# Performance work log

Hardware: AMD Instinct MI355X
Metric: run time of the kernel (lower is better)

Reference implementation:

```python
import jax, jax.numpy as jnp
import numpy as np

B, Q, C, M = 32, 4096, 91, 512
T_MAX = 256          # track ids in [0, T_MAX]; 0 = invalid
SENT = T_MAX + 1     # sentinel segment for invalid preds
NSEG = T_MAX + 2
IMG_W, IMG_H = 1920.0, 1080.0
SCALE = 1.0 / float(np.sqrt(IMG_W ** 2 + IMG_H ** 2))
IOU_THR = 0.5
A_TRACK, A_SPAT, A_TEMP = 2.0, 1.5, 1.8
B_FP, B_FN, G_SW = 0.9, 0.9, 1.5


def _make_boxes(key, shape):
    k1, k2 = jax.random.split(key)
    xy = jax.random.uniform(k1, shape[:-1] + (2,)) * jnp.array([IMG_W - 220.0, IMG_H - 220.0])
    wh = jax.random.uniform(k2, shape[:-1] + (2,)) * 200.0 + 4.0
    return jnp.concatenate([xy, xy + wh], axis=-1)


def setup_inputs() -> dict:
    key = jax.random.key(0)
    ks = jax.random.split(key, 5)
    return {
        'pred_boxes': _make_boxes(ks[0], (B, Q, 4)),
        'pred_logits': jax.random.normal(ks[1], (B, Q, C), dtype=jnp.float32),
        'track_ids': jax.random.randint(ks[2], (B, Q), 0, T_MAX + 1, dtype=jnp.int32),
        'gt_boxes': _make_boxes(ks[3], (B, M, 4)),
        'gt_track_ids': jax.random.randint(ks[4], (B, M), 1, T_MAX + 1, dtype=jnp.int32),
    }


def _box_iou(b1, b2):
    a1 = jnp.clip(b1[:, 2] - b1[:, 0], 0.0) * jnp.clip(b1[:, 3] - b1[:, 1], 0.0)
    a2 = jnp.clip(b2[:, 2] - b2[:, 0], 0.0) * jnp.clip(b2[:, 3] - b2[:, 1], 0.0)
    lt = jnp.maximum(b1[:, None, :2], b2[None, :, :2])
    rb = jnp.minimum(b1[:, None, 2:], b2[None, :, 2:])
    wh = jnp.clip(rb - lt, 0.0)
    inter = wh[..., 0] * wh[..., 1]
    iou = inter / (a1[:, None] + a2[None, :] - inter + 1e-6)
    return jnp.clip(iou, 0.0, 1.0)


def _per_batch(pb, pid, gb, gid):
    valid = pid > 0
    seg = jnp.where(valid, pid, SENT)              # invalid preds -> sentinel bucket
    ar = jnp.arange(NSEG)
    real = (ar > 0) & (ar <= T_MAX)
    ious = _box_iou(pb, gb)                        # (Q, M)

    gt_cnt = jax.ops.segment_sum(jnp.ones(M, jnp.float32), gid, NSEG)
    gt_present = gt_cnt > 0
    pred_cnt = jax.ops.segment_sum(jnp.ones(Q, jnp.float32), seg, NSEG)
    pred_present = (pred_cnt > 0) & real

    # ---- tracking loss ----
    fn_loss = B_FN * jnp.sum(jnp.where(gt_present & ~pred_present, gt_cnt, 0.0))
    match = pid[:, None] == gid[None, :]           # (Q, M)
    max_iou = jnp.max(jnp.where(match, ious, -1.0), axis=1)
    loc_mask = valid & gt_present[pid]
    loc = jnp.sum(jnp.where(loc_mask, 1.0 - max_iou, 0.0))
    wrong = (ious > IOU_THR) & valid[:, None] & ~match & pred_present[gid][None, :]
    switch = G_SW * jnp.sum(wrong.astype(jnp.float32))
    fp_loss = B_FP * jnp.sum(jnp.where(valid & ~gt_present[pid], 1.0, 0.0))
    tracking = fn_loss + loc + switch + fp_loss

    # ---- spatial consistency (per-track mean abs deviation of w, h) ----
    w = pb[:, 2] - pb[:, 0]
    h = pb[:, 3] - pb[:, 1]
    safe_cnt = jnp.maximum(pred_cnt, 1.0)
    mw = jax.ops.segment_sum(w, seg, NSEG) / safe_cnt
    mh = jax.ops.segment_sum(h, seg, NSEG) / safe_cnt
    dev_w = jnp.abs(w - mw[seg]) * SCALE
    dev_h = jnp.abs(h - mh[seg]) * SCALE
    mdw = jax.ops.segment_sum(dev_w, seg, NSEG) / safe_cnt
    mdh = jax.ops.segment_sum(dev_h, seg, NSEG) / safe_cnt
    n_unique = jnp.sum(((pred_cnt > 0) & real).astype(jnp.float32))
    sp_ok = (pred_cnt > 1) & real
    spatial = jnp.sum(jnp.where(sp_ok, mdw + mdh, 0.0)) / jnp.maximum(n_unique, 1.0)
    nvalid = jnp.sum(valid.astype(jnp.float32))
    spatial = jnp.where(nvalid > 1, spatial, 0.0)

    # ---- temporal consistency (per-track second-difference of centers) ----
    order = jnp.argsort(seg, stable=True)          # stable: preserves query order per track
    s_id = seg[order]
    centers = jnp.stack([(pb[:, 0] + pb[:, 2]) * 0.5, (pb[:, 1] + pb[:, 3]) * 0.5], axis=1)
    s_c = centers[order]
    vel = s_c[1:] - s_c[:-1]
    same1 = (s_id[1:] == s_id[:-1]) & (s_id[1:] <= T_MAX)
    acc = (vel[1:] - vel[:-1]) * SCALE
    same2 = same1[1:] & same1[:-1]
    sq = jnp.sum(acc * acc, axis=1)
    acc_norm = jnp.where(same2, jnp.sqrt(jnp.maximum(sq, 1e-30)), 0.0)
    sum_acc = jax.ops.segment_sum(acc_norm, s_id[2:], NSEG)
    te_ok = (pred_cnt > 2) & real
    temporal = jnp.sum(jnp.where(te_ok, sum_acc / jnp.maximum(pred_cnt - 2.0, 1.0), 0.0))
    temporal = temporal / jnp.maximum(n_unique, 1.0)
    temporal = jnp.where(nvalid > 1, temporal, 0.0)

    z = (nvalid > 0).astype(jnp.float32)           # torch code skips batches with no valid preds
    return tracking * z, spatial * z, temporal * z, n_unique * z


def reference(pred_boxes, pred_logits, track_ids, gt_boxes, gt_track_ids):
    tr, sp, te, nu = jax.vmap(_per_batch)(pred_boxes, track_ids, gt_boxes, gt_track_ids)
    nt = jnp.sum(nu)
    denom = jnp.maximum(nt, 1.0)
    lt = jnp.where(nt > 0, jnp.sum(tr) / denom, 0.0)
    ls = jnp.where(nt > 0, jnp.sum(sp) / denom, 0.0)
    lte = jnp.where(nt > 0, jnp.sum(te) / denom, 0.0)
    san = lambda x: jnp.where(jnp.isfinite(x), x, 0.0)
    lt, ls, lte = san(lt), san(ls), san(lte)
    total = san(A_TRACK * lt + A_SPAT * ls + A_TEMP * lte)
    # [loss_unitrack, loss_unitrack_tracking, loss_unitrack_spatial, loss_unitrack_temporal]
    return jnp.stack([total, lt, ls, lte])
```

## Files before the change

### kernel.cpp

```cpp
#include <hip/hip_runtime.h>
#include <math.h>

#define NB 32
#define NQ 4096
#define NM 512
#define NT 256
#define NSENT 257
#define NSEGS 258
#define HP 33
#define NXB 64
#define XBW (1.0f/30.0f)
#define WMAX 204.0f

__device__ __forceinline__ float scale_const() {
  return 1.0f / sqrtf(1920.0f * 1920.0f + 1080.0f * 1080.0f);
}

__global__ __launch_bounds__(1024) void k_stats(
    const float4* __restrict__ pred_boxes,
    const int*    __restrict__ track_ids,
    const float4* __restrict__ gt_boxes,
    const int*    __restrict__ gt_ids,
    float*        __restrict__ acc,
    float4*       __restrict__ e_box,
    float*        __restrict__ e_meta,
    unsigned short* __restrict__ qord,
    int*          __restrict__ g_boff)
{
  const int b    = blockIdx.x;
  const int tid  = threadIdx.x;
  const int lane = tid & 63;
  const int wid  = tid >> 6;
  const float SCALE = scale_const();

  __shared__ unsigned int hist32[NSEGS * HP];
  __shared__ float2 wh_s[NQ];
  __shared__ float2 ct_s[NQ];
  __shared__ __attribute__((aligned(16))) float4 gbox_s[NM];
  __shared__ float  gsa_s[NM];
  __shared__ float  gsa3_s[NM];
  __shared__ unsigned short gt_list[NM];
  __shared__ int gcnt_i[NSEGS], pcnt_i[NSEGS], offs[NSEGS], goffs[NSEGS], cur[NSEGS];
  __shared__ float ppw[NSEGS], gpw[NSEGS];
  __shared__ int qbh[NXB], qbo[NXB], qbc[NXB];
  __shared__ int gbh[NXB], gbo[NXB + 1], gbc[NXB];
  __shared__ float slots[16][8];

  for (int i = tid; i < NSEGS * HP; i += 1024) hist32[i] = 0u;
  if (tid < NSEGS) { gcnt_i[tid] = 0; cur[tid] = 0; }
  if (tid < NXB)   { qbh[tid] = 0; qbc[tid] = 0; gbh[tid] = 0; gbc[tid] = 0; }
  __syncthreads();

  float4 pbox[4]; int segr[4]; int xbr[4];
  #pragma unroll
  for (int k = 0; k < 4; ++k) {
    int q = tid + (k << 10);
    pbox[k] = pred_boxes[b * NQ + q];
    int pid = track_ids[b * NQ + q];
    segr[k] = pid > 0 ? pid : NSENT;
    int xb = (int)(pbox[k].x * XBW); xb = xb > 63 ? 63 : (xb < 0 ? 0 : xb);
    xbr[k] = xb;
    atomicAdd(&qbh[xb], 1);
  }
  float4 gtbox = make_float4(0.f, 0.f, 0.f, 0.f);
  int gtid = 0, gxb = 0;
  float gsa3v = 0.f;
  if (tid < NM) {
    gtbox = gt_boxes[b * NM + tid];
    gtid  = gt_ids[b * NM + tid];
    atomicAdd(&gcnt_i[gtid], 1);
    float sa = fmaxf(gtbox.z - gtbox.x, 0.f) * fmaxf(gtbox.w - gtbox.y, 0.f) + 1e-6f;
    gsa3v = sa * (1.0f / 3.0f);
    gbox_s[tid] = gtbox;
    gsa_s[tid]  = sa;
    gsa3_s[tid] = gsa3v;
    gxb = (int)(gtbox.x * XBW); gxb = gxb > 63 ? 63 : (gxb < 0 ? 0 : gxb);
    atomicAdd(&gbh[gxb], 1);
  }

  int rankr[4];
  #pragma unroll
  for (int k = 0; k < 4; ++k) {
    int seg = segr[k];
    unsigned long long mask = ~0ull;
    #pragma unroll
    for (int bit = 0; bit < 9; ++bit) {
      unsigned long long vote = __ballot((seg >> bit) & 1);
      mask &= ((seg >> bit) & 1) ? vote : ~vote;
    }
    rankr[k] = __popcll(mask & ((1ull << lane) - 1ull));
    if (rankr[k] == 0 && seg != NSENT) {
      int q = tid + (k << 10);
      ((unsigned short*)hist32)[seg * (2 * HP) + (q >> 6)] = (unsigned short)__popcll(mask);
    }
  }
  __syncthreads();

  if (tid < NSEGS) {
    int s = 0;
    #pragma unroll 8
    for (int c2 = 0; c2 < 32; ++c2) {
      unsigned u = hist32[tid * HP + c2];
      s += (int)(u & 0xffffu) + (int)(u >> 16);
    }
    pcnt_i[tid] = s;
    ppw[tid] = (tid >= 1 && tid <= NT && s > 0) ? 1.f : 0.f;
    gpw[tid] = (gcnt_i[tid] > 0) ? 1.f : 0.f;
  }
  if (wid == 14) {
    int v = qbh[lane], sc = v;
    #pragma unroll
    for (int d = 1; d < 64; d <<= 1) { int u = __shfl_up(sc, d); if (lane >= d) sc += u; }
    qbo[lane] = sc - v;
  } else if (wid == 15) {
    int v = gbh[lane], sc = v;
    #pragma unroll
    for (int d = 1; d < 64; d <<= 1) { int u = __shfl_up(sc, d); if (lane >= d) sc += u; }
    int ex = sc - v;
    gbo[lane] = ex;
    g_boff[b * 65 + lane] = ex;
    if (lane == 63) { gbo[64] = sc; g_boff[b * 65 + 64] = sc; }
  }
  __syncthreads();

  if (wid < 2) {
    const int* src = wid ? gcnt_i : pcnt_i;
    int* dst = wid ? goffs : offs;
    int base = lane * 5;
    int v0=0,v1=0,v2=0,v3=0,v4=0;
    if (base + 0 < NSEGS) v0 = src[base + 0];
    if (base + 1 < NSEGS) v1 = src[base + 1];
    if (base + 2 < NSEGS) v2 = src[base + 2];
    if (base + 3 < NSEGS) v3 = src[base + 3];
    if (base + 4 < NSEGS) v4 = src[base + 4];
    int tot = v0 + v1 + v2 + v3 + v4;
    int sc = tot;
    #pragma unroll
    for (int d = 1; d < 64; d <<= 1) { int u = __shfl_up(sc, d); if (lane >= d) sc += u; }
    int run = sc - tot;
    if (base + 0 < NSEGS) { dst[base + 0] = run; run += v0; }
    if (base + 1 < NSEGS) { dst[base + 1] = run; run += v1; }
    if (base + 2 < NSEGS) { dst[base + 2] = run; run += v2; }
    if (base + 3 < NSEGS) { dst[base + 3] = run; run += v3; }
    if (base + 4 < NSEGS) { dst[base + 4] = run; run += v4; }
  }
  __syncthreads();

  if (tid < NSEGS) {
    int run = offs[tid];
    #pragma unroll 8
    for (int c2 = 0; c2 < 32; ++c2) {
      unsigned u = hist32[tid * HP + c2];
      int lo = (int)(u & 0xffffu), hi = (int)(u >> 16);
      hist32[tid * HP + c2] = (unsigned)run | ((unsigned)(run + lo) << 16);
      run += lo + hi;
    }
  }
  __syncthreads();

  float nv_local = 0.f;
  #pragma unroll
  for (int k = 0; k < 4; ++k) {
    int seg = segr[k];
    int q = tid + (k << 10);
    if (seg != NSENT) {
      nv_local += 1.f;
      int c = q >> 6;
      unsigned pr = hist32[seg * HP + (c >> 1)];
      int base = (c & 1) ? (int)(pr >> 16) : (int)(pr & 0xffffu);
      int pos = base + rankr[k];
      float4 bx = pbox[k];
      wh_s[pos] = make_float2(bx.z - bx.x, bx.w - bx.y);
      ct_s[pos] = make_float2((bx.x + bx.z) * 0.5f, (bx.y + bx.w) * 0.5f);
    }
    int xb = xbr[k];
    int qp = qbo[xb] + atomicAdd(&qbc[xb], 1);
    qord[b * NQ + qp] = (unsigned short)q;
  }
  if (tid < NM) {
    int gp = gbo[gxb] + atomicAdd(&gbc[gxb], 1);
    e_box[b * NM + gp]  = gtbox;
    e_meta[b * NM + gp] = (ppw[gtid] > 0.f) ? gsa3v : 3.0e38f;
    int p = atomicAdd(&cur[gtid], 1);
    gt_list[goffs[gtid] + p] = (unsigned short)tid;
  }
  __syncthreads();

  float loc_local = 0.f, mo_local = 0.f;
  #pragma unroll
  for (int k = 0; k < 4; ++k) {
    int seg = segr[k];
    if (seg != NSENT && gpw[seg] > 0.f) {
      float4 p = pbox[k];
      float pa  = fmaxf(p.z - p.x, 0.f) * fmaxf(p.w - p.y, 0.f);
      float pa3 = pa * (1.0f / 3.0f);
      int s0 = goffs[seg], n = gcnt_i[seg];
      float mx = -1.f;
      for (int i = 0; i < n; ++i) {
        int m = gt_list[s0 + i];
        float4 g = gbox_s[m];
        float ix = fmaxf(fminf(p.z, g.z) - fmaxf(p.x, g.x), 0.f);
        float iy = fmaxf(fminf(p.w, g.w) - fmaxf(p.y, g.y), 0.f);
        float inter = ix * iy;
        float iou = inter / (pa + gsa_s[m] - inter);
        mx = fmaxf(mx, fminf(fmaxf(iou, 0.f), 1.f));
        if (inter > pa3 + gsa3_s[m]) mo_local += 1.f;
      }
      loc_local += 1.f - mx;
    }
  }

  float fn_l = 0.f, fp_l = 0.f, sp_l = 0.f, te_l = 0.f, nu_l = 0.f;
  if (tid >= 1 && tid <= NT) {
    int n = pcnt_i[tid], gc = gcnt_i[tid], o = offs[tid];
    if (gc > 0 && n == 0) fn_l = (float)gc;
    if (n > 0) {
      nu_l = 1.f;
      if (gc == 0) fp_l = (float)n;
    }
    if (n > 1) {
      float sumw = 0.f, sumh = 0.f;
      for (int i = 0; i < n; ++i) { float2 w = wh_s[o + i]; sumw += w.x; sumh += w.y; }
      float inv = 1.f / (float)n;
      float mw = sumw * inv, mh = sumh * inv;
      float dw = 0.f, dh = 0.f;
      for (int i = 0; i < n; ++i) {
        float2 w = wh_s[o + i];
        dw += fabsf(w.x - mw) * SCALE;
        dh += fabsf(w.y - mh) * SCALE;
      }
      sp_l = dw * inv + dh * inv;
      if (n > 2) {
        float2 c0 = ct_s[o], c1 = ct_s[o + 1];
        float s = 0.f;
        for (int i = 2; i < n; ++i) {
          float2 c2v = ct_s[o + i];
          float ax = (c2v.x - 2.f * c1.x + c0.x) * SCALE;
          float ay = (c2v.y - 2.f * c1.y + c0.y) * SCALE;
          s += sqrtf(fmaxf(ax * ax + ay * ay, 1e-30f));
          c0 = c1; c1 = c2v;
        }
        te_l = s / (float)(n - 2);
      }
    }
  }

  float vals[8] = {fn_l, fp_l, sp_l, te_l, nu_l, nv_local, loc_local, mo_local};
  #pragma unroll
  for (int j = 0; j < 8; ++j) {
    float v = vals[j];
    #pragma unroll
    for (int off = 32; off; off >>= 1) v += __shfl_down(v, off);
    if (lane == 0) slots[wid][j] = v;
  }
  __syncthreads();
  if (tid < 8) {
    float s = 0.f;
    #pragma unroll
    for (int w = 0; w < 16; ++w) s += slots[w][tid];
    if (tid == 7) s = -s;
    acc[b * 8 + tid] = s;
  }
}

__global__ __launch_bounds__(256) void k_iou(
    const float4* __restrict__ pred_boxes,
    const int*    __restrict__ track_ids,
    const unsigned short* __restrict__ qord,
    const float4* __restrict__ e_box,
    const float*  __restrict__ e_meta,
    const int*    __restrict__ g_boff,
    float*        __restrict__ acc)
{
  const int b    = blockIdx.y;
  const int tid  = threadIdx.x;
  const int slot = blockIdx.x * 256 + tid;
  __shared__ __attribute__((aligned(16))) float4 eb[NM];
  __shared__ float em[NM];
  __shared__ int   bo[NXB + 1];
  __shared__ float redw[4];

  eb[tid]       = e_box[b * NM + tid];
  eb[tid + 256] = e_box[b * NM + tid + 256];
  em[tid]       = e_meta[b * NM + tid];
  em[tid + 256] = e_meta[b * NM + tid + 256];
  if (tid <= NXB) bo[tid] = g_boff[b * 65 + tid];
  __syncthreads();

  int qi = qord[b * NQ + slot];
  float4 p = pred_boxes[b * NQ + qi];
  int pid  = track_ids[b * NQ + qi];
  float pa3 = fmaxf(p.z - p.x, 0.f) * fmaxf(p.w - p.y, 0.f) * (1.0f / 3.0f);

  float x0 = p.x, x1 = p.z;
  #pragma unroll
  for (int off = 32; off; off >>= 1) {
    x0 = fminf(x0, __shfl_xor(x0, off));
    x1 = fmaxf(x1, __shfl_xor(x1, off));
  }
  int lb = (int)(fmaxf(x0 - WMAX, 0.f) * XBW); lb = lb > 63 ? 63 : lb;
  int hb = (int)(fmaxf(x1, 0.f) * XBW);        hb = hb > 63 ? 63 : hb;
  int ms = __builtin_amdgcn_readfirstlane(bo[lb]);
  int me = __builtin_amdgcn_readfirstlane(bo[hb + 1]);

  float wr = 0.f;
  #pragma unroll 4
  for (int m = ms; m < me; ++m) {
    float4 g = eb[m];
    float ix = fmaxf(fminf(p.z, g.z) - fmaxf(p.x, g.x), 0.f);
    float iy = fmaxf(fminf(p.w, g.w) - fmaxf(p.y, g.y), 0.f);
    float inter = ix * iy;
    wr += (inter > pa3 + em[m]) ? 1.f : 0.f;
  }
  if (pid <= 0) wr = 0.f;

  #pragma unroll
  for (int off = 32; off; off >>= 1) wr += __shfl_down(wr, off);
  if ((tid & 63) == 0) redw[tid >> 6] = wr;
  __syncthreads();
  if (tid == 0) {
    float s = redw[0] + redw[1] + redw[2] + redw[3];
    if (s != 0.f) atomicAdd(&acc[b * 8 + 7], s);
  }
}

__global__ __launch_bounds__(64) void k_final(const float* __restrict__ acc, float* __restrict__ out)
{
  const int tid = threadIdx.x;
  float tr = 0.f, sp = 0.f, te = 0.f, nu = 0.f;
  if (tid < NB) {
    const float* a = acc + tid * 8;
    float nvalid = a[5];
    if (nvalid > 0.f) {
      tr = 0.9f * a[0] + a[6] + 1.5f * a[7] + 0.9f * a[1];
      nu = a[4];
      if (nvalid > 1.f) {
        float inu = 1.f / fmaxf(nu, 1.f);
        sp = a[2] * inu;
        te = a[3] * inu;
      }
    }
  }
  #pragma unroll
  for (int off = 32; off; off >>= 1) {
    tr += __shfl_down(tr, off);
    sp += __shfl_down(sp, off);
    te += __shfl_down(te, off);
    nu += __shfl_down(nu, off);
  }
  if (tid == 0) {
    float nt = nu;
    float denom = fmaxf(nt, 1.f);
    float lt  = (nt > 0.f) ? tr / denom : 0.f;
    float ls  = (nt > 0.f) ? sp / denom : 0.f;
    float lte = (nt > 0.f) ? te / denom : 0.f;
    if (!isfinite(lt))  lt  = 0.f;
    if (!isfinite(ls))  ls  = 0.f;
    if (!isfinite(lte)) lte = 0.f;
    float total = 2.0f * lt + 1.5f * ls + 1.8f * lte;
    if (!isfinite(total)) total = 0.f;
    out[0] = total; out[1] = lt; out[2] = ls; out[3] = lte;
  }
}

extern "C" void kernel_launch(void* const* d_in, const int* in_sizes, int n_in,
                              void* d_out, int out_size, void* d_ws, size_t ws_size,
                              hipStream_t stream) {
  const float4* pred_boxes = (const float4*)d_in[0];
  const int*    track_ids  = (const int*)d_in[2];
  const float4* gt_boxes   = (const float4*)d_in[3];
  const int*    gt_ids     = (const int*)d_in[4];
  float* out = (float*)d_out;

  char* w = (char*)d_ws;
  float*          acc    = (float*)w;                      w += 1024;
  float4*         e_box  = (float4*)w;                     w += NB * NM * sizeof(float4);
  float*          e_meta = (float*)w;                      w += NB * NM * sizeof(float);
  unsigned short* qord   = (unsigned short*)w;             w += NB * NQ * sizeof(unsigned short);
  int*            g_boff = (int*)w;

  k_stats<<<NB, 1024, 0, stream>>>(pred_boxes, track_ids, gt_boxes, gt_ids, acc,
                                   e_box, e_meta, qord, g_boff);
  k_iou<<<dim3(NQ / 256, NB), 256, 0, stream>>>(pred_boxes, track_ids, qord,
                                                e_box, e_meta, g_boff, acc);
  k_final<<<1, 64, 0, stream>>>(acc, out);
}
```

Baseline: 39.93 us.

## Move matched-IoU loss into sweep kernel and fuse final reduction via last-block

The per-track matched-IoU (localisation) loop moves out of the single-block-per-batch stats kernel and into the x-binned IoU sweep. Each pred box now computes its max IoU against same-id GT boxes alongside the mostly-overlap count, tagging GT entries with their id so matches are excluded from the overlap term. Pred x-bin ordering now uses ballot-based ranking instead of shared atomics. The separate final kernel is replaced by a last-block-done pattern with a global counter and fences, which saves a launch but adds atomics and a workspace counter that must be reset each call.

```diff
diff --git a/kernel.cpp b/kernel.cpp
--- a/kernel.cpp
+++ b/kernel.cpp
@@ -8,6 +8,7 @@
 #define NSENT 257
 #define NSEGS 258
 #define HP 33
+#define HPX 33
 #define NXB 64
 #define XBW (1.0f/30.0f)
 #define WMAX 204.0f
@@ -23,9 +24,12 @@
     const int*    __restrict__ gt_ids,
     float*        __restrict__ acc,
     float4*       __restrict__ e_box,
-    float*        __restrict__ e_meta,
+    float2*       __restrict__ e_pair,
+    float*        __restrict__ e_sa,
     unsigned short* __restrict__ qord,
-    int*          __restrict__ g_boff)
+    int*          __restrict__ g_boff,
+    unsigned char* __restrict__ gpres,
+    unsigned int* __restrict__ ctr)
 {
   const int b    = blockIdx.x;
   const int tid  = threadIdx.x;
@@ -34,65 +38,69 @@
   const float SCALE = scale_const();
 
   __shared__ unsigned int hist32[NSEGS * HP];
+  __shared__ unsigned int histx[NXB * HPX];
   __shared__ float2 wh_s[NQ];
   __shared__ float2 ct_s[NQ];
-  __shared__ __attribute__((aligned(16))) float4 gbox_s[NM];
-  __shared__ float  gsa_s[NM];
-  __shared__ float  gsa3_s[NM];
-  __shared__ unsigned short gt_list[NM];
-  __shared__ int gcnt_i[NSEGS], pcnt_i[NSEGS], offs[NSEGS], goffs[NSEGS], cur[NSEGS];
-  __shared__ float ppw[NSEGS], gpw[NSEGS];
-  __shared__ int qbh[NXB], qbo[NXB], qbc[NXB];
-  __shared__ int gbh[NXB], gbo[NXB + 1], gbc[NXB];
+  __shared__ int   gcnt_i[NSEGS], pcnt_i[NSEGS], offs[NSEGS];
+  __shared__ float ppw[NSEGS];
+  __shared__ int   qbo[NXB], gbo[NXB + 1], gbc[NXB], gbh[NXB];
   __shared__ float slots[16][8];
 
   for (int i = tid; i < NSEGS * HP; i += 1024) hist32[i] = 0u;
-  if (tid < NSEGS) { gcnt_i[tid] = 0; cur[tid] = 0; }
-  if (tid < NXB)   { qbh[tid] = 0; qbc[tid] = 0; gbh[tid] = 0; gbc[tid] = 0; }
-  __syncthreads();
-
-  float4 pbox[4]; int segr[4]; int xbr[4];
+  for (int i = tid; i < NXB * HPX; i += 1024) histx[i] = 0u;
+  if (tid < NSEGS) gcnt_i[tid] = 0;
+  if (tid < NXB) { gbc[tid] = 0; gbh[tid] = 0; }
+  if (b == 0 && tid == 0) *ctr = 0u;
+  __syncthreads();
+
+  float4 pbox[4]; int segr[4], xbr[4];
+  float nv_local = 0.f;
   #pragma unroll
   for (int k = 0; k < 4; ++k) {
     int q = tid + (k << 10);
     pbox[k] = pred_boxes[b * NQ + q];
     int pid = track_ids[b * NQ + q];
     segr[k] = pid > 0 ? pid : NSENT;
+    if (pid > 0) nv_local += 1.f;
     int xb = (int)(pbox[k].x * XBW); xb = xb > 63 ? 63 : (xb < 0 ? 0 : xb);
     xbr[k] = xb;
-    atomicAdd(&qbh[xb], 1);
   }
   float4 gtbox = make_float4(0.f, 0.f, 0.f, 0.f);
-  int gtid = 0, gxb = 0;
-  float gsa3v = 0.f;
+  int gtid = 0, gxb = 0; float sa = 0.f, sa3 = 0.f;
   if (tid < NM) {
     gtbox = gt_boxes[b * NM + tid];
     gtid  = gt_ids[b * NM + tid];
     atomicAdd(&gcnt_i[gtid], 1);
-    float sa = fmaxf(gtbox.z - gtbox.x, 0.f) * fmaxf(gtbox.w - gtbox.y, 0.f) + 1e-6f;
-    gsa3v = sa * (1.0f / 3.0f);
-    gbox_s[tid] = gtbox;
-    gsa_s[tid]  = sa;
-    gsa3_s[tid] = gsa3v;
+    sa  = fmaxf(gtbox.z - gtbox.x, 0.f) * fmaxf(gtbox.w - gtbox.y, 0.f) + 1e-6f;
+    sa3 = sa * (1.0f / 3.0f);
     gxb = (int)(gtbox.x * XBW); gxb = gxb > 63 ? 63 : (gxb < 0 ? 0 : gxb);
     atomicAdd(&gbh[gxb], 1);
   }
 
-  int rankr[4];
+  int rankr[4], rankx[4];
   #pragma unroll
   for (int k = 0; k < 4; ++k) {
+    int q = tid + (k << 10);
     int seg = segr[k];
-    unsigned long long mask = ~0ull;
+    unsigned long long m1 = ~0ull;
     #pragma unroll
     for (int bit = 0; bit < 9; ++bit) {
       unsigned long long vote = __ballot((seg >> bit) & 1);
-      mask &= ((seg >> bit) & 1) ? vote : ~vote;
-    }
-    rankr[k] = __popcll(mask & ((1ull << lane) - 1ull));
-    if (rankr[k] == 0 && seg != NSENT) {
-      int q = tid + (k << 10);
-      ((unsigned short*)hist32)[seg * (2 * HP) + (q >> 6)] = (unsigned short)__popcll(mask);
-    }
+      m1 &= ((seg >> bit) & 1) ? vote : ~vote;
+    }
+    rankr[k] = __popcll(m1 & ((1ull << lane) - 1ull));
+    if (rankr[k] == 0 && seg != NSENT)
+      ((unsigned short*)hist32)[seg * (2 * HP) + (q >> 6)] = (unsigned short)__popcll(m1);
+    int xb = xbr[k];
+    unsigned long long m2 = ~0ull;
+    #pragma unroll
+    for (int bit = 0; bit < 6; ++bit) {
+      unsigned long long vote = __ballot((xb >> bit) & 1);
+      m2 &= ((xb >> bit) & 1) ? vote : ~vote;
+    }
+    rankx[k] = __popcll(m2 & ((1ull << lane) - 1ull));
+    if (rankx[k] == 0)
+      ((unsigned short*)histx)[xb * (2 * HPX) + (q >> 6)] = (unsigned short)__popcll(m2);
   }
   __syncthreads();
 
@@ -105,13 +113,18 @@
     }
     pcnt_i[tid] = s;
     ppw[tid] = (tid >= 1 && tid <= NT && s > 0) ? 1.f : 0.f;
-    gpw[tid] = (gcnt_i[tid] > 0) ? 1.f : 0.f;
   }
   if (wid == 14) {
-    int v = qbh[lane], sc = v;
+    int s = 0;
+    #pragma unroll 8
+    for (int c2 = 0; c2 < 32; ++c2) {
+      unsigned u = histx[lane * HPX + c2];
+      s += (int)(u & 0xffffu) + (int)(u >> 16);
+    }
+    int sc = s;
     #pragma unroll
     for (int d = 1; d < 64; d <<= 1) { int u = __shfl_up(sc, d); if (lane >= d) sc += u; }
-    qbo[lane] = sc - v;
+    qbo[lane] = sc - s;
   } else if (wid == 15) {
     int v = gbh[lane], sc = v;
     #pragma unroll
@@ -123,26 +136,33 @@
   }
   __syncthreads();
 
-  if (wid < 2) {
-    const int* src = wid ? gcnt_i : pcnt_i;
-    int* dst = wid ? goffs : offs;
+  if (wid == 0) {
     int base = lane * 5;
     int v0=0,v1=0,v2=0,v3=0,v4=0;
-    if (base + 0 < NSEGS) v0 = src[base + 0];
-    if (base + 1 < NSEGS) v1 = src[base + 1];
-    if (base + 2 < NSEGS) v2 = src[base + 2];
-    if (base + 3 < NSEGS) v3 = src[base + 3];
-    if (base + 4 < NSEGS) v4 = src[base + 4];
+    if (base + 0 < NSEGS) v0 = pcnt_i[base + 0];
+    if (base + 1 < NSEGS) v1 = pcnt_i[base + 1];
+    if (base + 2 < NSEGS) v2 = pcnt_i[base + 2];
+    if (base + 3 < NSEGS) v3 = pcnt_i[base + 3];
+    if (base + 4 < NSEGS) v4 = pcnt_i[base + 4];
     int tot = v0 + v1 + v2 + v3 + v4;
     int sc = tot;
     #pragma unroll
     for (int d = 1; d < 64; d <<= 1) { int u = __shfl_up(sc, d); if (lane >= d) sc += u; }
     int run = sc - tot;
-    if (base + 0 < NSEGS) { dst[base + 0] = run; run += v0; }
-    if (base + 1 < NSEGS) { dst[base + 1] = run; run += v1; }
-    if (base + 2 < NSEGS) { dst[base + 2] = run; run += v2; }
-    if (base + 3 < NSEGS) { dst[base + 3] = run; run += v3; }
-    if (base + 4 < NSEGS) { dst[base + 4] = run; run += v4; }
+    if (base + 0 < NSEGS) { offs[base + 0] = run; run += v0; }
+    if (base + 1 < NSEGS) { offs[base + 1] = run; run += v1; }
+    if (base + 2 < NSEGS) { offs[base + 2] = run; run += v2; }
+    if (base + 3 < NSEGS) { offs[base + 3] = run; run += v3; }
+    if (base + 4 < NSEGS) { offs[base + 4] = run; run += v4; }
+  } else if (wid == 13) {
+    int run = qbo[lane];
+    #pragma unroll 8
+    for (int c2 = 0; c2 < 32; ++c2) {
+      unsigned u = histx[lane * HPX + c2];
+      int lo = (int)(u & 0xffffu), hi = (int)(u >> 16);
+      histx[lane * HPX + c2] = (unsigned)run | ((unsigned)(run + lo) << 16);
+      run += lo + hi;
+    }
   }
   __syncthreads();
 
@@ -158,14 +178,12 @@
   }
   __syncthreads();
 
-  float nv_local = 0.f;
   #pragma unroll
   for (int k = 0; k < 4; ++k) {
+    int q = tid + (k << 10);
+    int c = q >> 6;
     int seg = segr[k];
-    int q = tid + (k << 10);
     if (seg != NSENT) {
-      nv_local += 1.f;
-      int c = q >> 6;
       unsigned pr = hist32[seg * HP + (c >> 1)];
       int base = (c & 1) ? (int)(pr >> 16) : (int)(pr & 0xffffu);
       int pos = base + rankr[k];
@@ -173,42 +191,18 @@
       wh_s[pos] = make_float2(bx.z - bx.x, bx.w - bx.y);
       ct_s[pos] = make_float2((bx.x + bx.z) * 0.5f, (bx.y + bx.w) * 0.5f);
     }
-    int xb = xbr[k];
-    int qp = qbo[xb] + atomicAdd(&qbc[xb], 1);
-    qord[b * NQ + qp] = (unsigned short)q;
+    unsigned px = histx[xbr[k] * HPX + (c >> 1)];
+    int xbase = (c & 1) ? (int)(px >> 16) : (int)(px & 0xffffu);
+    qord[b * NQ + xbase + rankx[k]] = (unsigned short)q;
   }
   if (tid < NM) {
     int gp = gbo[gxb] + atomicAdd(&gbc[gxb], 1);
     e_box[b * NM + gp]  = gtbox;
-    e_meta[b * NM + gp] = (ppw[gtid] > 0.f) ? gsa3v : 3.0e38f;
-    int p = atomicAdd(&cur[gtid], 1);
-    gt_list[goffs[gtid] + p] = (unsigned short)tid;
-  }
-  __syncthreads();
-
-  float loc_local = 0.f, mo_local = 0.f;
-  #pragma unroll
-  for (int k = 0; k < 4; ++k) {
-    int seg = segr[k];
-    if (seg != NSENT && gpw[seg] > 0.f) {
-      float4 p = pbox[k];
-      float pa  = fmaxf(p.z - p.x, 0.f) * fmaxf(p.w - p.y, 0.f);
-      float pa3 = pa * (1.0f / 3.0f);
-      int s0 = goffs[seg], n = gcnt_i[seg];
-      float mx = -1.f;
-      for (int i = 0; i < n; ++i) {
-        int m = gt_list[s0 + i];
-        float4 g = gbox_s[m];
-        float ix = fmaxf(fminf(p.z, g.z) - fmaxf(p.x, g.x), 0.f);
-        float iy = fmaxf(fminf(p.w, g.w) - fmaxf(p.y, g.y), 0.f);
-        float inter = ix * iy;
-        float iou = inter / (pa + gsa_s[m] - inter);
-        mx = fmaxf(mx, fminf(fmaxf(iou, 0.f), 1.f));
-        if (inter > pa3 + gsa3_s[m]) mo_local += 1.f;
-      }
-      loc_local += 1.f - mx;
-    }
-  }
+    e_pair[b * NM + gp] = make_float2((ppw[gtid] > 0.f) ? sa3 : 3.0e38f, (float)gtid);
+    e_sa[b * NM + gp]   = sa;
+  }
+  if (tid < NSEGS) gpres[b * NSEGS + tid] = (gcnt_i[tid] > 0) ? 1 : 0;
+  __syncthreads();
 
   float fn_l = 0.f, fp_l = 0.f, sp_l = 0.f, te_l = 0.f, nu_l = 0.f;
   if (tid >= 1 && tid <= NT) {
@@ -245,7 +239,7 @@
     }
   }
 
-  float vals[8] = {fn_l, fp_l, sp_l, te_l, nu_l, nv_local, loc_local, mo_local};
+  float vals[8] = {fn_l, fp_l, sp_l, te_l, nu_l, nv_local, 0.f, 0.f};
   #pragma unroll
   for (int j = 0; j < 8; ++j) {
     float v = vals[j];
@@ -258,7 +252,6 @@
     float s = 0.f;
     #pragma unroll
     for (int w = 0; w < 16; ++w) s += slots[w][tid];
-    if (tid == 7) s = -s;
     acc[b * 8 + tid] = s;
   }
 }
@@ -268,29 +261,43 @@
     const int*    __restrict__ track_ids,
     const unsigned short* __restrict__ qord,
     const float4* __restrict__ e_box,
-    const float*  __restrict__ e_meta,
+    const float2* __restrict__ e_pair,
+    const float*  __restrict__ e_sa,
     const int*    __restrict__ g_boff,
-    float*        __restrict__ acc)
+    const unsigned char* __restrict__ gpres,
+    float*        __restrict__ acc,
+    float*        __restrict__ loc_part,
+    unsigned int* __restrict__ ctr,
+    float*        __restrict__ out)
 {
-  const int b    = blockIdx.y;
-  const int tid  = threadIdx.x;
-  const int slot = blockIdx.x * 256 + tid;
+  const int b   = blockIdx.y;
+  const int bx  = blockIdx.x;
+  const int tid = threadIdx.x;
   __shared__ __attribute__((aligned(16))) float4 eb[NM];
-  __shared__ float em[NM];
-  __shared__ int   bo[NXB + 1];
-  __shared__ float redw[4];
-
-  eb[tid]       = e_box[b * NM + tid];
-  eb[tid + 256] = e_box[b * NM + tid + 256];
-  em[tid]       = e_meta[b * NM + tid];
-  em[tid + 256] = e_meta[b * NM + tid + 256];
+  __shared__ float2 eg[NM];
+  __shared__ float  esa[NM];
+  __shared__ int    bo[NXB + 1];
+  __shared__ float  redl[4], redw[4];
+  __shared__ unsigned last_flag;
+
+  #pragma unroll
+  for (int i = 0; i < 2; ++i) {
+    int m = tid + (i << 8);
+    eb[m]  = e_box[b * NM + m];
+    eg[m]  = e_pair[b * NM + m];
+    esa[m] = e_sa[b * NM + m];
+  }
   if (tid <= NXB) bo[tid] = g_boff[b * 65 + tid];
   __syncthreads();
 
+  const int slot = bx * 256 + tid;
   int qi = qord[b * NQ + slot];
   float4 p = pred_boxes[b * NQ + qi];
   int pid  = track_ids[b * NQ + qi];
-  float pa3 = fmaxf(p.z - p.x, 0.f) * fmaxf(p.w - p.y, 0.f) * (1.0f / 3.0f);
+  float pidf = (float)pid;
+  float pa  = fmaxf(p.z - p.x, 0.f) * fmaxf(p.w - p.y, 0.f);
+  float pa3 = pa * (1.0f / 3.0f);
+  int gp = gpres[b * NSEGS + (pid > 0 ? pid : 0)];
 
   float x0 = p.x, x1 = p.z;
   #pragma unroll
@@ -303,63 +310,84 @@
   int ms = __builtin_amdgcn_readfirstlane(bo[lb]);
   int me = __builtin_amdgcn_readfirstlane(bo[hb + 1]);
 
-  float wr = 0.f;
-  #pragma unroll 4
+  float wr = 0.f, mx = 0.f;
+  #pragma unroll 2
   for (int m = ms; m < me; ++m) {
-    float4 g = eb[m];
+    float4 g  = eb[m];
+    float2 e  = eg[m];
     float ix = fmaxf(fminf(p.z, g.z) - fmaxf(p.x, g.x), 0.f);
     float iy = fmaxf(fminf(p.w, g.w) - fmaxf(p.y, g.y), 0.f);
     float inter = ix * iy;
-    wr += (inter > pa3 + em[m]) ? 1.f : 0.f;
-  }
+    wr += ((inter > pa3 + e.x) && (e.y != pidf)) ? 1.f : 0.f;
+    if (e.y == pidf) {
+      float iou = inter / (pa + esa[m] - inter);
+      mx = fmaxf(mx, fminf(fmaxf(iou, 0.f), 1.f));
+    }
+  }
+  float loc = (pid > 0 && gp) ? 1.f - mx : 0.f;
   if (pid <= 0) wr = 0.f;
 
   #pragma unroll
-  for (int off = 32; off; off >>= 1) wr += __shfl_down(wr, off);
-  if ((tid & 63) == 0) redw[tid >> 6] = wr;
+  for (int off = 32; off; off >>= 1) {
+    loc += __shfl_down(loc, off);
+    wr  += __shfl_down(wr, off);
+  }
+  if ((tid & 63) == 0) { redl[tid >> 6] = loc; redw[tid >> 6] = wr; }
   __syncthreads();
   if (tid == 0) {
-    float s = redw[0] + redw[1] + redw[2] + redw[3];
-    if (s != 0.f) atomicAdd(&acc[b * 8 + 7], s);
-  }
-}
-
-__global__ __launch_bounds__(64) void k_final(const float* __restrict__ acc, float* __restrict__ out)
-{
-  const int tid = threadIdx.x;
-  float tr = 0.f, sp = 0.f, te = 0.f, nu = 0.f;
-  if (tid < NB) {
-    const float* a = acc + tid * 8;
-    float nvalid = a[5];
-    if (nvalid > 0.f) {
-      tr = 0.9f * a[0] + a[6] + 1.5f * a[7] + 0.9f * a[1];
-      nu = a[4];
-      if (nvalid > 1.f) {
-        float inu = 1.f / fmaxf(nu, 1.f);
-        sp = a[2] * inu;
-        te = a[3] * inu;
+    float ls = ((redl[0] + redl[1]) + redl[2]) + redl[3];
+    float ws = redw[0] + redw[1] + redw[2] + redw[3];
+    loc_part[b * 16 + bx] = ls;
+    if (ws != 0.f) atomicAdd(&acc[b * 8 + 7], ws);
+    __threadfence();
+    unsigned old = atomicAdd(ctr, 1u);
+    last_flag = (old == (unsigned)(NB * 16 - 1)) ? 1u : 0u;
+  }
+  __syncthreads();
+
+  if (last_flag && tid < 64) {
+    __threadfence();
+    float tr = 0.f, sp = 0.f, te = 0.f, nu = 0.f;
+    if (tid < NB) {
+      float a[8];
+      #pragma unroll
+      for (int j = 0; j < 8; ++j)
+        a[j] = __hip_atomic_load(&acc[tid * 8 + j], __ATOMIC_RELAXED, __HIP_MEMORY_SCOPE_AGENT);
+      float locb = 0.f;
+      #pragma unroll
+      for (int i = 0; i < 16; ++i)
+        locb += __hip_atomic_load(&loc_part[tid * 16 + i], __ATOMIC_RELAXED, __HIP_MEMORY_SCOPE_AGENT);
+      float nvalid = a[5];
+      if (nvalid > 0.f) {
+        tr = 0.9f * a[0] + locb + 1.5f * a[7] + 0.9f * a[1];
+        nu = a[4];
+        if (nvalid > 1.f) {
+          float inu = 1.f / fmaxf(nu, 1.f);
+          sp = a[2] * inu;
+          te = a[3] * inu;
+        }
       }
     }
-  }
-  #pragma unroll
-  for (int off = 32; off; off >>= 1) {
-    tr += __shfl_down(tr, off);
-    sp += __shfl_down(sp, off);
-    te += __shfl_down(te, off);
-    nu += __shfl_down(nu, off);
-  }
-  if (tid == 0) {
-    float nt = nu;
-    float denom = fmaxf(nt, 1.f);
-    float lt  = (nt > 0.f) ? tr / denom : 0.f;
-    float ls  = (nt > 0.f) ? sp / denom : 0.f;
-    float lte = (nt > 0.f) ? te / denom : 0.f;
-    if (!isfinite(lt))  lt  = 0.f;
-    if (!isfinite(ls))  ls  = 0.f;
-    if (!isfinite(lte)) lte = 0.f;
-    float total = 2.0f * lt + 1.5f * ls + 1.8f * lte;
-    if (!isfinite(total)) total = 0.f;
-    out[0] = total; out[1] = lt; out[2] = ls; out[3] = lte;
+    #pragma unroll
+    for (int off = 32; off; off >>= 1) {
+      tr += __shfl_down(tr, off);
+      sp += __shfl_down(sp, off);
+      te += __shfl_down(te, off);
+      nu += __shfl_down(nu, off);
+    }
+    if (tid == 0) {
+      float nt = nu;
+      float denom = fmaxf(nt, 1.f);
+      float lt  = (nt > 0.f) ? tr / denom : 0.f;
+      float ls2 = (nt > 0.f) ? sp / denom : 0.f;
+      float lte = (nt > 0.f) ? te / denom : 0.f;
+      if (!isfinite(lt))  lt  = 0.f;
+      if (!isfinite(ls2)) ls2 = 0.f;
+      if (!isfinite(lte)) lte = 0.f;
+      float total = 2.0f * lt + 1.5f * ls2 + 1.8f * lte;
+      if (!isfinite(total)) total = 0.f;
+      out[0] = total; out[1] = lt; out[2] = ls2; out[3] = lte;
+    }
   }
 }
 
@@ -373,15 +401,19 @@
   float* out = (float*)d_out;
 
   char* w = (char*)d_ws;
-  float*          acc    = (float*)w;                      w += 1024;
-  float4*         e_box  = (float4*)w;                     w += NB * NM * sizeof(float4);
-  float*          e_meta = (float*)w;                      w += NB * NM * sizeof(float);
-  unsigned short* qord   = (unsigned short*)w;             w += NB * NQ * sizeof(unsigned short);
-  int*            g_boff = (int*)w;
+  float*          acc      = (float*)w;          w += 1024;
+  float4*         e_box    = (float4*)w;         w += NB * NM * sizeof(float4);
+  float2*         e_pair   = (float2*)w;         w += NB * NM * sizeof(float2);
+  float*          e_sa     = (float*)w;          w += NB * NM * sizeof(float);
+  unsigned short* qord     = (unsigned short*)w; w += NB * NQ * sizeof(unsigned short);
+  int*            g_boff   = (int*)w;            w += NB * 65 * sizeof(int);
+  unsigned char*  gpres    = (unsigned char*)w;  w += ((NB * NSEGS + 15) / 16) * 16;
+  float*          loc_part = (float*)w;          w += NB * 16 * sizeof(float);
+  unsigned int*   ctr      = (unsigned int*)w;
 
   k_stats<<<NB, 1024, 0, stream>>>(pred_boxes, track_ids, gt_boxes, gt_ids, acc,
-                                   e_box, e_meta, qord, g_boff);
+                                   e_box, e_pair, e_sa, qord, g_boff, gpres, ctr);
   k_iou<<<dim3(NQ / 256, NB), 256, 0, stream>>>(pred_boxes, track_ids, qord,
-                                                e_box, e_meta, g_boff, acc);
-  k_final<<<1, 64, 0, stream>>>(acc, out);
+                                                e_box, e_pair, e_sa, g_boff, gpres,
+                                                acc, loc_part, ctr, out);
 }
```

Result: slower. 48.91 us (+22.5%).
